# Performance work log

Measured on AMD Instinct MI355X. Metric: run time of the kernel, lower is better.

## Reference

```python
import jax, jax.numpy as jnp
import numpy as np

N, IN_DIM, LDIM = 8192, 512, 256
NEG_SLOPE = 0.01  # torch F.leaky_relu default
EPS = 1e-10


def setup_inputs() -> dict:
    key = jax.random.key(0)
    k1, k2, k3, k4 = jax.random.split(key, 4)
    x = jax.random.normal(k1, (N, IN_DIM), dtype=jnp.float32)
    adj = jax.random.uniform(k2, (N, N), dtype=jnp.float32)
    # nn.Linear(in_dim, learning_dim, bias=False) weight: [learning_dim, in_dim]
    proj_w = jax.random.normal(k3, (LDIM, IN_DIM), dtype=jnp.float32) * (1.0 / np.sqrt(IN_DIM))
    # nn.init.uniform_(learn_w, a=0, b=1)
    learn_w = jax.random.uniform(k4, (LDIM,), dtype=jnp.float32)
    return {"x": x, "adj": adj, "proj_w": proj_w, "learn_w": learn_w}


def reference(x, adj, proj_w, learn_w):
    # x_hat = projection(x): [N, LDIM]
    x_hat = x @ proj_w.T
    # cosine-distance score: sum_d w_d * (1 - xn_i[d] * xn_j[d])
    #   = sum(w) - (xn * w) @ xn.T  -- avoids the N x N x D intermediate
    xn = x_hat / jnp.linalg.norm(x_hat, axis=-1, keepdims=True)  # [N, LDIM]
    scores = jnp.sum(learn_w) - jnp.einsum('id,jd->ij', xn * learn_w, xn)  # [N, N]
    out = jax.nn.leaky_relu(scores, NEG_SLOPE)
    out = out - jnp.max(out, axis=-1, keepdims=True)
    soft_adj = adj * jnp.exp(out)
    soft_adj = soft_adj / jnp.sum(soft_adj, axis=-1, keepdims=True) + EPS
    return soft_adj
```

## Files before the change

kernel.cpp:

```cpp
#include <hip/hip_runtime.h>
#include <stdint.h>

#define NN 8192
#define KDIM 512
#define LDIM 256

typedef short bf16x8 __attribute__((ext_vector_type(8)));
typedef float f32x4 __attribute__((ext_vector_type(4)));

__device__ __forceinline__ unsigned short f2bf(float f) {
  unsigned int u = __float_as_uint(f);
  u = (u + 0x7fffu + ((u >> 16) & 1u)) >> 16;
  return (unsigned short)u;
}

__device__ __forceinline__ void async_ld16(const unsigned short* g, unsigned short* l) {
  __builtin_amdgcn_global_load_lds(
      (const __attribute__((address_space(1))) unsigned int*)g,
      (__attribute__((address_space(3))) unsigned int*)l, 16, 0, 0);
}

__global__ __launch_bounds__(256) void cast_kernel(
    const float* __restrict__ x, const float* __restrict__ pw,
    unsigned short* __restrict__ xb, unsigned short* __restrict__ pwb) {
  int i = blockIdx.x * 256 + threadIdx.x;
  xb[i] = f2bf(x[i]);
  if (i < LDIM * KDIM) pwb[i] = f2bf(pw[i]);
}

__global__ __launch_bounds__(256) void norm_kernel(
    const float* __restrict__ xh, const float* __restrict__ w,
    unsigned short* __restrict__ Ab, unsigned short* __restrict__ Bb) {
  const int row = blockIdx.x;
  const int d = threadIdx.x;
  const float v = xh[row * LDIM + d];
  float ss = v * v;
#pragma unroll
  for (int m = 1; m < 64; m <<= 1) ss += __shfl_xor(ss, m);
  __shared__ float s4[4];
  if ((d & 63) == 0) s4[d >> 6] = ss;
  __syncthreads();
  const float tot = s4[0] + s4[1] + s4[2] + s4[3];
  const float inv = 1.0f / sqrtf(tot);
  const float xn = v * inv;
  Bb[row * LDIM + d] = f2bf(xn);
  Ab[row * LDIM + d] = f2bf(xn * w[d]);
}

template <int K, bool EPI>
__global__ __launch_bounds__(256) void gemm_bt(
    const unsigned short* __restrict__ A,
    const unsigned short* __restrict__ B,
    float* __restrict__ C,
    const float* __restrict__ adj,
    float* __restrict__ rowsum,
    int ldC) {
  __shared__ unsigned short As[128 * 32];
  __shared__ unsigned short Bs[128 * 32];
  __shared__ float rs[128];

  const int tid = threadIdx.x;
  const int wave = tid >> 6;
  const int lane = tid & 63;
  const int quad = lane >> 4;
  const int l16 = lane & 15;
  const int wm = wave >> 1;
  const int wn = wave & 1;

  if (EPI && tid < 128) rs[tid] = 0.0f;

  const size_t row0 = (size_t)blockIdx.y * 128;
  const size_t col0 = (size_t)blockIdx.x * 128;

  const int c0 = wave * 128 + lane;
  const int mA = c0 >> 2;
  const int kA = (c0 & 3) * 8;
  const unsigned short* Ag = A + (row0 + mA) * (size_t)K + kA;
  const unsigned short* Bg = B + (col0 + mA) * (size_t)K + kA;
  char* AsB = (char*)As;
  char* BsB = (char*)Bs;
  unsigned short* dA0 = (unsigned short*)(AsB + wave * 2048);
  unsigned short* dA1 = (unsigned short*)(AsB + wave * 2048 + 1024);
  unsigned short* dB0 = (unsigned short*)(BsB + wave * 2048);
  unsigned short* dB1 = (unsigned short*)(BsB + wave * 2048 + 1024);

  f32x4 acc[4][4];
#pragma unroll
  for (int i = 0; i < 4; ++i)
#pragma unroll
    for (int j = 0; j < 4; ++j) acc[i][j] = (f32x4)(0.0f);

  for (int k0 = 0; k0 < K; k0 += 32) {
    async_ld16(Ag + k0, dA0);
    async_ld16(Ag + 16 * (size_t)K + k0, dA1);
    async_ld16(Bg + k0, dB0);
    async_ld16(Bg + 16 * (size_t)K + k0, dB1);
    __syncthreads();

    bf16x8 av[4], bv[4];
#pragma unroll
    for (int mt = 0; mt < 4; ++mt)
      av[mt] = *(const bf16x8*)(AsB + (wm * 64 + mt * 16 + l16) * 64 + quad * 16);
#pragma unroll
    for (int nt = 0; nt < 4; ++nt)
      bv[nt] = *(const bf16x8*)(BsB + (wn * 64 + nt * 16 + l16) * 64 + quad * 16);
#pragma unroll
    for (int mt = 0; mt < 4; ++mt)
#pragma unroll
      for (int nt = 0; nt < 4; ++nt)
        acc[mt][nt] = __builtin_amdgcn_mfma_f32_16x16x32_bf16(av[mt], bv[nt], acc[mt][nt], 0, 0, 0);
    __syncthreads();
  }

  if (!EPI) {
#pragma unroll
    for (int mt = 0; mt < 4; ++mt)
#pragma unroll
      for (int nt = 0; nt < 4; ++nt)
#pragma unroll
        for (int r = 0; r < 4; ++r) {
          size_t gr = row0 + wm * 64 + mt * 16 + quad * 4 + r;
          size_t gc = col0 + wn * 64 + nt * 16 + l16;
          C[gr * (size_t)ldC + gc] = acc[mt][nt][r];
        }
  } else {
#pragma unroll
    for (int mt = 0; mt < 4; ++mt) {
      float rsum[4] = {0.f, 0.f, 0.f, 0.f};
#pragma unroll
      for (int nt = 0; nt < 4; ++nt) {
#pragma unroll
        for (int r = 0; r < 4; ++r) {
          size_t gr = row0 + wm * 64 + mt * 16 + quad * 4 + r;
          size_t gc = col0 + wn * 64 + nt * 16 + l16;
          size_t idx = gr * (size_t)ldC + gc;
          float t = adj[idx] * __expf(-acc[mt][nt][r]);
          C[idx] = t;
          rsum[r] += t;
        }
      }
#pragma unroll
      for (int r = 0; r < 4; ++r) {
        float v = rsum[r];
        v += __shfl_xor(v, 1);
        v += __shfl_xor(v, 2);
        v += __shfl_xor(v, 4);
        v += __shfl_xor(v, 8);
        if (l16 == 0) atomicAdd(&rs[wm * 64 + mt * 16 + quad * 4 + r], v);
      }
    }
    __syncthreads();
    if (tid < 128) atomicAdd(&rowsum[row0 + tid], rs[tid]);
  }
}

__global__ __launch_bounds__(256) void scale_kernel(
    float* __restrict__ t, const float* __restrict__ rowsum) {
  const size_t i = (size_t)blockIdx.x * 256 + threadIdx.x;
  const int row = (int)(i >> 11);
  float4 v = ((float4*)t)[i];
  const float inv = 1.0f / rowsum[row];
  v.x = v.x * inv + 1e-10f;
  v.y = v.y * inv + 1e-10f;
  v.z = v.z * inv + 1e-10f;
  v.w = v.w * inv + 1e-10f;
  ((float4*)t)[i] = v;
}

extern "C" void kernel_launch(void* const* d_in, const int* in_sizes, int n_in,
                              void* d_out, int out_size, void* d_ws, size_t ws_size,
                              hipStream_t stream) {
  (void)in_sizes; (void)n_in; (void)out_size; (void)ws_size;
  const float* x   = (const float*)d_in[0];
  const float* adj = (const float*)d_in[1];
  const float* pw  = (const float*)d_in[2];
  const float* lw  = (const float*)d_in[3];
  float* out = (float*)d_out;
  char* ws = (char*)d_ws;

  unsigned short* xb   = (unsigned short*)(ws);
  unsigned short* pwb  = (unsigned short*)(ws + 8388608);
  float*          xhat = (float*)(ws + 8650752);
  unsigned short* Ab   = (unsigned short*)(ws + 17039360);
  unsigned short* Bb   = (unsigned short*)(ws + 21233664);
  float*          rsum = (float*)(ws + 25427968);

  cast_kernel<<<(NN * KDIM) / 256, 256, 0, stream>>>(x, pw, xb, pwb);
  gemm_bt<KDIM, false><<<dim3(2, 64), 256, 0, stream>>>(xb, pwb, xhat, nullptr, nullptr, LDIM);
  norm_kernel<<<NN, 256, 0, stream>>>(xhat, lw, Ab, Bb);
  hipMemsetAsync(rsum, 0, NN * sizeof(float), stream);
  gemm_bt<LDIM, true><<<dim3(64, 64), 256, 0, stream>>>(Ab, Bb, out, adj, rsum, NN);
  scale_kernel<<<(NN / 4) * (NN / 256), 256, 0, stream>>>(out, rsum);
}
```

Baseline: 618.9 us.

## Stage epilogue through LDS for coalesced writes and store bf16 intermediate

The GEMM epilogue now transposes accumulator tiles through shared memory so each thread reads adj and writes output as contiguous float4 vectors, replacing scattered scalar accesses. When the workspace is large enough, the unnormalized exp*adj values go to a bf16 buffer instead of the fp32 output, which halves the intermediate write and the scale kernel's read. The scale kernel then expands bf16 to fp32 output. This costs precision in the stored intermediate, and the row sums are computed from the rounded values. It also adds extra syncthreads per mt step.

```diff
diff --git a/kernel.cpp b/kernel.cpp
--- a/kernel.cpp
+++ b/kernel.cpp
@@ -6,12 +6,16 @@
 #define LDIM 256
 
 typedef short bf16x8 __attribute__((ext_vector_type(8)));
+typedef short short8 __attribute__((ext_vector_type(8)));
 typedef float f32x4 __attribute__((ext_vector_type(4)));
 
 __device__ __forceinline__ unsigned short f2bf(float f) {
   unsigned int u = __float_as_uint(f);
   u = (u + 0x7fffu + ((u >> 16) & 1u)) >> 16;
   return (unsigned short)u;
+}
+__device__ __forceinline__ float bf2f(unsigned short s) {
+  return __uint_as_float(((unsigned int)s) << 16);
 }
 
 __device__ __forceinline__ void async_ld16(const unsigned short* g, unsigned short* l) {
@@ -47,11 +51,12 @@
   Ab[row * LDIM + d] = f2bf(xn * w[d]);
 }
 
-template <int K, bool EPI>
+template <int K, int MODE>
 __global__ __launch_bounds__(256) void gemm_bt(
     const unsigned short* __restrict__ A,
     const unsigned short* __restrict__ B,
     float* __restrict__ C,
+    unsigned short* __restrict__ T,
     const float* __restrict__ adj,
     float* __restrict__ rowsum,
     int ldC) {
@@ -66,8 +71,6 @@
   const int l16 = lane & 15;
   const int wm = wave >> 1;
   const int wn = wave & 1;
-
-  if (EPI && tid < 128) rs[tid] = 0.0f;
 
   const size_t row0 = (size_t)blockIdx.y * 128;
   const size_t col0 = (size_t)blockIdx.x * 128;
@@ -112,7 +115,7 @@
     __syncthreads();
   }
 
-  if (!EPI) {
+  if constexpr (MODE == 0) {
 #pragma unroll
     for (int mt = 0; mt < 4; ++mt)
 #pragma unroll
@@ -124,37 +127,88 @@
           C[gr * (size_t)ldC + gc] = acc[mt][nt][r];
         }
   } else {
+    __shared__ float trans[32 * 132];
+    const int s = tid >> 3;
+    const int cb = tid & 7;
+    const int coff = cb * 16;
 #pragma unroll
     for (int mt = 0; mt < 4; ++mt) {
-      float rsum[4] = {0.f, 0.f, 0.f, 0.f};
-#pragma unroll
-      for (int nt = 0; nt < 4; ++nt) {
-#pragma unroll
-        for (int r = 0; r < 4; ++r) {
-          size_t gr = row0 + wm * 64 + mt * 16 + quad * 4 + r;
-          size_t gc = col0 + wn * 64 + nt * 16 + l16;
-          size_t idx = gr * (size_t)ldC + gc;
-          float t = adj[idx] * __expf(-acc[mt][nt][r]);
-          C[idx] = t;
-          rsum[r] += t;
+      __syncthreads();
+#pragma unroll
+      for (int nt = 0; nt < 4; ++nt)
+#pragma unroll
+        for (int r = 0; r < 4; ++r)
+          trans[(wm * 16 + quad * 4 + r) * 132 + wn * 64 + nt * 16 + l16] =
+              acc[mt][nt][r];
+      __syncthreads();
+      const size_t gr = row0 + (size_t)(s >> 4) * 64 + mt * 16 + (s & 15);
+      const float* arow = adj + gr * NN + col0 + coff;
+      float av16[16];
+#pragma unroll
+      for (int q = 0; q < 4; ++q) {
+        float4 a4 = ((const float4*)arow)[q];
+        av16[q * 4 + 0] = a4.x;
+        av16[q * 4 + 1] = a4.y;
+        av16[q * 4 + 2] = a4.z;
+        av16[q * 4 + 3] = a4.w;
+      }
+      const float* drow = &trans[s * 132 + coff];
+      float part = 0.0f;
+      if constexpr (MODE == 1) {
+        short8 p0, p1;
+#pragma unroll
+        for (int j = 0; j < 16; ++j) {
+          float tv = av16[j] * __expf(-drow[j]);
+          unsigned short us = f2bf(tv);
+          part += bf2f(us);
+          if (j < 8) p0[j] = (short)us; else p1[j - 8] = (short)us;
         }
+        short8* trow = (short8*)(T + gr * NN + col0 + coff);
+        trow[0] = p0;
+        trow[1] = p1;
+      } else {
+        float4 o[4];
+#pragma unroll
+        for (int j = 0; j < 16; ++j) {
+          float tv = av16[j] * __expf(-drow[j]);
+          part += tv;
+          ((float*)o)[j] = tv;
+        }
+        float4* crow = (float4*)(C + gr * NN + col0 + coff);
+#pragma unroll
+        for (int q = 0; q < 4; ++q) crow[q] = o[q];
       }
-#pragma unroll
-      for (int r = 0; r < 4; ++r) {
-        float v = rsum[r];
-        v += __shfl_xor(v, 1);
-        v += __shfl_xor(v, 2);
-        v += __shfl_xor(v, 4);
-        v += __shfl_xor(v, 8);
-        if (l16 == 0) atomicAdd(&rs[wm * 64 + mt * 16 + quad * 4 + r], v);
-      }
+      part += __shfl_xor(part, 1);
+      part += __shfl_xor(part, 2);
+      part += __shfl_xor(part, 4);
+      if (cb == 0) rs[(s >> 4) * 64 + mt * 16 + (s & 15)] = part;
     }
     __syncthreads();
     if (tid < 128) atomicAdd(&rowsum[row0 + tid], rs[tid]);
   }
 }
 
-__global__ __launch_bounds__(256) void scale_kernel(
+__global__ __launch_bounds__(256) void scale_bf16_kernel(
+    const unsigned short* __restrict__ T, const float* __restrict__ rowsum,
+    float* __restrict__ out) {
+  const size_t i = (size_t)blockIdx.x * 256 + threadIdx.x;
+  const int row = (int)(i >> 10);
+  short8 tv = ((const short8*)T)[i];
+  const float inv = 1.0f / rowsum[row];
+  float4 o0, o1;
+  o0.x = bf2f((unsigned short)tv[0]) * inv + 1e-10f;
+  o0.y = bf2f((unsigned short)tv[1]) * inv + 1e-10f;
+  o0.z = bf2f((unsigned short)tv[2]) * inv + 1e-10f;
+  o0.w = bf2f((unsigned short)tv[3]) * inv + 1e-10f;
+  o1.x = bf2f((unsigned short)tv[4]) * inv + 1e-10f;
+  o1.y = bf2f((unsigned short)tv[5]) * inv + 1e-10f;
+  o1.z = bf2f((unsigned short)tv[6]) * inv + 1e-10f;
+  o1.w = bf2f((unsigned short)tv[7]) * inv + 1e-10f;
+  ((float4*)out)[i * 2] = o0;
+  ((float4*)out)[i * 2 + 1] = o1;
+}
+
+__global__ __launch_bounds__(256) void scale_f32_kernel(
     float* __restrict__ t, const float* __restrict__ rowsum) {
   const size_t i = (size_t)blockIdx.x * 256 + threadIdx.x;
   const int row = (int)(i >> 11);
@@ -170,7 +224,7 @@
 extern "C" void kernel_launch(void* const* d_in, const int* in_sizes, int n_in,
                               void* d_out, int out_size, void* d_ws, size_t ws_size,
                               hipStream_t stream) {
-  (void)in_sizes; (void)n_in; (void)out_size; (void)ws_size;
+  (void)in_sizes; (void)n_in; (void)out_size;
   const float* x   = (const float*)d_in[0];
   const float* adj = (const float*)d_in[1];
   const float* pw  = (const float*)d_in[2];
@@ -184,11 +238,18 @@
   unsigned short* Ab   = (unsigned short*)(ws + 17039360);
   unsigned short* Bb   = (unsigned short*)(ws + 21233664);
   float*          rsum = (float*)(ws + 25427968);
+  unsigned short* Tbuf = (unsigned short*)(ws + 25460736);
+  const bool big_ws = ws_size >= 25460736ull + (size_t)NN * NN * 2ull;
 
   cast_kernel<<<(NN * KDIM) / 256, 256, 0, stream>>>(x, pw, xb, pwb);
-  gemm_bt<KDIM, false><<<dim3(2, 64), 256, 0, stream>>>(xb, pwb, xhat, nullptr, nullptr, LDIM);
+  gemm_bt<KDIM, 0><<<dim3(2, 64), 256, 0, stream>>>(xb, pwb, xhat, nullptr, nullptr, nullptr, LDIM);
   norm_kernel<<<NN, 256, 0, stream>>>(xhat, lw, Ab, Bb);
   hipMemsetAsync(rsum, 0, NN * sizeof(float), stream);
-  gemm_bt<LDIM, true><<<dim3(64, 64), 256, 0, stream>>>(Ab, Bb, out, adj, rsum, NN);
-  scale_kernel<<<(NN / 4) * (NN / 256), 256, 0, stream>>>(out, rsum);
-}
+  if (big_ws) {
+    gemm_bt<LDIM, 1><<<dim3(64, 64), 256, 0, stream>>>(Ab, Bb, nullptr, Tbuf, adj, rsum, NN);
+    scale_bf16_kernel<<<(NN / 8) * (NN / 256), 256, 0, stream>>>(Tbuf, rsum, out);
+  } else {
+    gemm_bt<LDIM, 2><<<dim3(64, 64), 256, 0, stream>>>(Ab, Bb, out, nullptr, adj, rsum, NN);
+    scale_f32_kernel<<<(NN / 4) * (NN / 256), 256, 0, stream>>>(out, rsum);
+  }
+}
```

Result: faster. 542.3 us (-12.4%).
